# Kernel tuning notes

Hardware: AMD Instinct MI355X
Metric: run time of the kernel (lower is better)

Reference implementation:

```python
import jax, jax.numpy as jnp
import numpy as np

B, C, H, W = 32, 17, 96, 72
K = 3
DIL = 1
PAD = (K // 2) * DIL
KK = K * K


def setup_inputs() -> dict:
    key = jax.random.key(0)
    k1, k2, k3, k4, k5 = jax.random.split(key, 5)
    x = jax.random.normal(k1, (B, C, H, W), jnp.float32)
    offsets = jax.random.normal(k2, (B, 2 * C * KK, H, W), jnp.float32)
    mask = jax.random.uniform(k3, (B, C * KK, H, W), jnp.float32)
    # depthwise conv: weight [C_out=C, C_in/groups=1, K, K], bias [C]
    weight = jax.random.normal(k4, (C, 1, K, K), jnp.float32) * 0.1
    bias = jax.random.normal(k5, (C,), jnp.float32) * 0.01
    return {"x": x, "offsets": offsets, "mask": mask, "weight": weight, "bias": bias}


def _deform_conv(x, offsets, mask, weight, bias):
    # Modulated deformable conv (DCNv2), depthwise, offset_groups == channels.
    off = offsets.reshape(B, C, KK, 2, H, W)
    dy = off[:, :, :, 0]  # [B,C,KK,H,W]
    dx = off[:, :, :, 1]
    m = mask.reshape(B, C, KK, H, W)

    ky, kx = jnp.meshgrid(jnp.arange(K), jnp.arange(K), indexing="ij")
    ky = ky.reshape(KK)
    kx = kx.reshape(KK)
    hh = jnp.arange(H)
    ww = jnp.arange(W)
    # base sampling grid [KK,H,W]
    base_y = (-PAD + ky[:, None, None] * DIL + hh[None, :, None] + 0 * ww[None, None, :]).astype(jnp.float32)
    base_x = (-PAD + kx[:, None, None] * DIL + 0 * hh[None, :, None] + ww[None, None, :]).astype(jnp.float32)

    py = base_y[None, None] + dy  # [B,C,KK,H,W]
    px = base_x[None, None] + dx

    y0f = jnp.floor(py)
    x0f = jnp.floor(px)
    wy = py - y0f
    wx = px - x0f
    y0 = y0f.astype(jnp.int32)
    x0 = x0f.astype(jnp.int32)

    img = x.reshape(B, C, H * W)

    def corner(yi, xi, w):
        # zero-padding semantics: out-of-bounds corners contribute 0
        valid = (yi >= 0) & (yi < H) & (xi >= 0) & (xi < W)
        idx = jnp.clip(yi, 0, H - 1) * W + jnp.clip(xi, 0, W - 1)
        v = jnp.take_along_axis(img, idx.reshape(B, C, -1), axis=2).reshape(B, C, KK, H, W)
        return v * jnp.where(valid, w, 0.0)

    val = (corner(y0, x0, (1 - wy) * (1 - wx))
           + corner(y0, x0 + 1, (1 - wy) * wx)
           + corner(y0 + 1, x0, wy * (1 - wx))
           + corner(y0 + 1, x0 + 1, wy * wx))

    out = jnp.einsum("bckhw,ck->bchw", val * m, weight.reshape(C, KK))
    return out + bias[None, :, None, None]


def reference(x, offsets, mask, weight, bias):
    return _deform_conv(x, offsets, mask, weight, bias)
```

## Files before the change

### kernel.cpp

```cpp
#include <hip/hip_runtime.h>

#define Bn   32
#define Cn   17
#define Hn   96
#define Wn   72
#define Kn   3
#define KKn  9
#define PADn 1
#define HWn  (Hn * Wn)

__global__ __launch_bounds__(256) void deform_conv_kernel(
    const float* __restrict__ x,
    const float* __restrict__ offsets,
    const float* __restrict__ mask,
    const float* __restrict__ weight,
    const float* __restrict__ bias,
    float* __restrict__ out)
{
    const int hw = blockIdx.x * blockDim.x + threadIdx.x;
    const int bc = blockIdx.y;
    if (hw >= HWn) return;

    const int c = bc % Cn;
    const int h = hw / Wn;
    const int w = hw - h * Wn;

    const float* __restrict__ xp   = x       + (size_t)bc * HWn;
    const float* __restrict__ offp = offsets + (size_t)bc * (KKn * 2 * HWn) + hw;
    const float* __restrict__ mp   = mask    + (size_t)bc * (KKn * HWn) + hw;
    const float* __restrict__ wp   = weight  + c * KKn;

    float acc = bias[c];

    #pragma unroll
    for (int kk = 0; kk < KKn; ++kk) {
        const int ky = kk / Kn;
        const int kx = kk - ky * Kn;

        const float dy = offp[(size_t)(kk * 2 + 0) * HWn];
        const float dx = offp[(size_t)(kk * 2 + 1) * HWn];
        const float m  = mp[(size_t)kk * HWn];

        const float py = (float)(h - PADn + ky) + dy;
        const float px = (float)(w - PADn + kx) + dx;

        const float y0f = floorf(py);
        const float x0f = floorf(px);
        const float wy  = py - y0f;
        const float wx  = px - x0f;
        const int y0 = (int)y0f;
        const int x0 = (int)x0f;
        const int y1 = y0 + 1;
        const int x1 = x0 + 1;

        const int y0c = min(max(y0, 0), Hn - 1);
        const int y1c = min(max(y1, 0), Hn - 1);
        const int x0c = min(max(x0, 0), Wn - 1);
        const int x1c = min(max(x1, 0), Wn - 1);

        const bool vy0 = (y0 >= 0) & (y0 < Hn);
        const bool vy1 = (y1 >= 0) & (y1 < Hn);
        const bool vx0 = (x0 >= 0) & (x0 < Wn);
        const bool vx1 = (x1 >= 0) & (x1 < Wn);

        const float w00 = (vy0 & vx0) ? (1.f - wy) * (1.f - wx) : 0.f;
        const float w01 = (vy0 & vx1) ? (1.f - wy) * wx         : 0.f;
        const float w10 = (vy1 & vx0) ? wy * (1.f - wx)         : 0.f;
        const float w11 = (vy1 & vx1) ? wy * wx                 : 0.f;

        float v = 0.f;
        v += xp[y0c * Wn + x0c] * w00;
        v += xp[y0c * Wn + x1c] * w01;
        v += xp[y1c * Wn + x0c] * w10;
        v += xp[y1c * Wn + x1c] * w11;

        acc += v * m * wp[kk];
    }

    out[(size_t)bc * HWn + hw] = acc;
}

extern "C" void kernel_launch(void* const* d_in, const int* in_sizes, int n_in,
                              void* d_out, int out_size, void* d_ws, size_t ws_size,
                              hipStream_t stream) {
    const float* x       = (const float*)d_in[0];
    const float* offsets = (const float*)d_in[1];
    const float* mask    = (const float*)d_in[2];
    const float* weight  = (const float*)d_in[3];
    const float* bias    = (const float*)d_in[4];
    float* out = (float*)d_out;

    dim3 block(256, 1, 1);
    dim3 grid((HWn + 255) / 256, Bn * Cn, 1);
    deform_conv_kernel<<<grid, block, 0, stream>>>(x, offsets, mask, weight, bias, out);
}
```

Baseline: 479.1 us.

## Stage input plane in LDS and process four pixels per thread with vector loads

Each block copies its full (b,c) input plane into shared memory and performs the bilinear gathers from LDS instead of global memory. Threads now handle four consecutive pixels, using float4 loads for offsets and mask and a float4 store for the output. This is meant to cut global gather latency and load instruction count, at the cost of redundantly loading each plane once per block (nine blocks per plane) and using 27 KB of LDS per block, which limits occupancy.

```diff
diff --git a/kernel.cpp b/kernel.cpp
--- a/kernel.cpp
+++ b/kernel.cpp
@@ -8,8 +8,10 @@
 #define KKn  9
 #define PADn 1
 #define HWn  (Hn * Wn)
+#define PX_PER_BLOCK 768
+#define NBLK_X (HWn / PX_PER_BLOCK)
 
-__global__ __launch_bounds__(256) void deform_conv_kernel(
+__global__ __launch_bounds__(192) void deform_conv_kernel(
     const float* __restrict__ x,
     const float* __restrict__ offsets,
     const float* __restrict__ mask,
@@ -17,67 +19,91 @@
     const float* __restrict__ bias,
     float* __restrict__ out)
 {
-    const int hw = blockIdx.x * blockDim.x + threadIdx.x;
-    const int bc = blockIdx.y;
-    if (hw >= HWn) return;
+    __shared__ float xs[HWn];
 
-    const int c = bc % Cn;
-    const int h = hw / Wn;
-    const int w = hw - h * Wn;
+    const int tid = threadIdx.x;
+    const int bc  = blockIdx.y;
+    const int c   = bc % Cn;
 
-    const float* __restrict__ xp   = x       + (size_t)bc * HWn;
+    {
+        const float4* __restrict__ xp4 = (const float4*)(x + (size_t)bc * HWn);
+        float4* xs4 = (float4*)xs;
+        #pragma unroll
+        for (int j = 0; j < HWn / 4 / 192; ++j) {
+            const int i = j * 192 + tid;
+            xs4[i] = xp4[i];
+        }
+    }
+    __syncthreads();
+
+    const int hw = blockIdx.x * PX_PER_BLOCK + tid * 4;
+    const int h  = hw / Wn;
+    const int w  = hw - h * Wn;
+
     const float* __restrict__ offp = offsets + (size_t)bc * (KKn * 2 * HWn) + hw;
     const float* __restrict__ mp   = mask    + (size_t)bc * (KKn * HWn) + hw;
     const float* __restrict__ wp   = weight  + c * KKn;
 
-    float acc = bias[c];
+    const float bv = bias[c];
+    float acc[4] = {bv, bv, bv, bv};
 
     #pragma unroll
     for (int kk = 0; kk < KKn; ++kk) {
+        const float4 dy4 = *(const float4*)(offp + (size_t)(kk * 2 + 0) * HWn);
+        const float4 dx4 = *(const float4*)(offp + (size_t)(kk * 2 + 1) * HWn);
+        const float4 m4  = *(const float4*)(mp + (size_t)kk * HWn);
+        const float  wk  = wp[kk];
+
         const int ky = kk / Kn;
         const int kx = kk - ky * Kn;
+        const float base_y = (float)(h - PADn + ky);
 
-        const float dy = offp[(size_t)(kk * 2 + 0) * HWn];
-        const float dx = offp[(size_t)(kk * 2 + 1) * HWn];
-        const float m  = mp[(size_t)kk * HWn];
+        #pragma unroll
+        for (int p = 0; p < 4; ++p) {
+            const float dy = ((const float*)&dy4)[p];
+            const float dx = ((const float*)&dx4)[p];
+            const float m  = ((const float*)&m4)[p];
 
-        const float py = (float)(h - PADn + ky) + dy;
-        const float px = (float)(w - PADn + kx) + dx;
+            const float py = base_y + dy;
+            const float px = (float)(w + p - PADn + kx) + dx;
 
-        const float y0f = floorf(py);
-        const float x0f = floorf(px);
-        const float wy  = py - y0f;
-        const float wx  = px - x0f;
-        const int y0 = (int)y0f;
-        const int x0 = (int)x0f;
-        const int y1 = y0 + 1;
-        const int x1 = x0 + 1;
+            const float y0f = floorf(py);
+            const float x0f = floorf(px);
+            const float wy  = py - y0f;
+            const float wx  = px - x0f;
+            const int y0 = (int)y0f;
+            const int x0 = (int)x0f;
+            const int y1 = y0 + 1;
+            const int x1 = x0 + 1;
 
-        const int y0c = min(max(y0, 0), Hn - 1);
-        const int y1c = min(max(y1, 0), Hn - 1);
-        const int x0c = min(max(x0, 0), Wn - 1);
-        const int x1c = min(max(x1, 0), Wn - 1);
+            const int y0c = min(max(y0, 0), Hn - 1);
+            const int y1c = min(max(y1, 0), Hn - 1);
+            const int x0c = min(max(x0, 0), Wn - 1);
+            const int x1c = min(max(x1, 0), Wn - 1);
 
-        const bool vy0 = (y0 >= 0) & (y0 < Hn);
-        const bool vy1 = (y1 >= 0) & (y1 < Hn);
-        const bool vx0 = (x0 >= 0) & (x0 < Wn);
-        const bool vx1 = (x1 >= 0) & (x1 < Wn);
+            const bool vy0 = (y0 >= 0) & (y0 < Hn);
+            const bool vy1 = (y1 >= 0) & (y1 < Hn);
+            const bool vx0 = (x0 >= 0) & (x0 < Wn);
+            const bool vx1 = (x1 >= 0) & (x1 < Wn);
 
-        const float w00 = (vy0 & vx0) ? (1.f - wy) * (1.f - wx) : 0.f;
-        const float w01 = (vy0 & vx1) ? (1.f - wy) * wx         : 0.f;
-        const float w10 = (vy1 & vx0) ? wy * (1.f - wx)         : 0.f;
-        const float w11 = (vy1 & vx1) ? wy * wx                 : 0.f;
+            const float w00 = (vy0 & vx0) ? (1.f - wy) * (1.f - wx) : 0.f;
+            const float w01 = (vy0 & vx1) ? (1.f - wy) * wx         : 0.f;
+            const float w10 = (vy1 & vx0) ? wy * (1.f - wx)         : 0.f;
+            const float w11 = (vy1 & vx1) ? wy * wx                 : 0.f;
 
-        float v = 0.f;
-        v += xp[y0c * Wn + x0c] * w00;
-        v += xp[y0c * Wn + x1c] * w01;
-        v += xp[y1c * Wn + x0c] * w10;
-        v += xp[y1c * Wn + x1c] * w11;
+            float v = 0.f;
+            v += xs[y0c * Wn + x0c] * w00;
+            v += xs[y0c * Wn + x1c] * w01;
+            v += xs[y1c * Wn + x0c] * w10;
+            v += xs[y1c * Wn + x1c] * w11;
 
-        acc += v * m * wp[kk];
+            acc[p] += v * m * wk;
+        }
     }
 
-    out[(size_t)bc * HWn + hw] = acc;
+    float4 o;
+    o.x = acc[0]; o.y = acc[1]; o.z = acc[2]; o.w = acc[3];
+    *(float4*)(out + (size_t)bc * HWn + hw) = o;
 }
 
 extern "C" void kernel_launch(void* const* d_in, const int* in_sizes, int n_in,
@@ -90,7 +116,7 @@
     const float* bias    = (const float*)d_in[4];
     float* out = (float*)d_out;
 
-    dim3 block(256, 1, 1);
-    dim3 grid((HWn + 255) / 256, Bn * Cn, 1);
+    dim3 block(192, 1, 1);
+    dim3 grid(NBLK_X, Bn * Cn, 1);
     deform_conv_kernel<<<grid, block, 0, stream>>>(x, offsets, mask, weight, bias, out);
 }
```

Result: faster. 461.4 us (-3.7%).
